# Performance work log

Hardware: AMD Instinct MI355X
Metric: run time of the kernel (lower is better)

The kernel has to match this reference:

```python
import jax, jax.numpy as jnp
import numpy as np

D_MODEL = 512
HIDDEN = 2 * D_MODEL
B, L = 8, 2048
R_MIN, R_MAX = 0.8, 0.99
LN_EPS = 1e-5


def setup_inputs() -> dict:
    key = jax.random.key(0)
    ks = jax.random.split(key, 12)
    x = jax.random.normal(ks[0], (B, L, D_MODEL), jnp.float32)
    mask = jnp.ones((B, L), jnp.float32)
    # LRU eigenvalue init, exactly as the torch __init__
    u1 = jax.random.uniform(ks[1], (HIDDEN,), jnp.float32)
    u2 = jax.random.uniform(ks[2], (HIDDEN,), jnp.float32)
    nu_log = jnp.log(-0.5 * jnp.log(u1 * (R_MAX ** 2 - R_MIN ** 2) + R_MIN ** 2))
    theta_log = jnp.log(u2 * 2.0 * np.pi)
    diag_lambda = jnp.exp(jax.lax.complex(-jnp.exp(nu_log), jnp.exp(theta_log)))
    gamma_log = jnp.log(jnp.sqrt(1.0 - jnp.abs(diag_lambda) ** 2))
    params_log = jnp.stack([nu_log, theta_log, gamma_log])  # (3, HIDDEN)
    s_in = 1.0 / np.sqrt(D_MODEL)
    s_out = 1.0 / np.sqrt(HIDDEN)
    # complex Linear weights (real+imag parts; trained weights are fully complex)
    W_in_re = jax.random.uniform(ks[3], (HIDDEN, D_MODEL), jnp.float32, -s_in, s_in)
    W_in_im = jax.random.uniform(ks[4], (HIDDEN, D_MODEL), jnp.float32, -s_in, s_in)
    b_in_re = jax.random.uniform(ks[5], (HIDDEN,), jnp.float32, -s_in, s_in)
    b_in_im = jax.random.uniform(ks[6], (HIDDEN,), jnp.float32, -s_in, s_in)
    W_out_re = jax.random.uniform(ks[7], (D_MODEL, HIDDEN), jnp.float32, -s_out, s_out)
    W_out_im = jax.random.uniform(ks[8], (D_MODEL, HIDDEN), jnp.float32, -s_out, s_out)
    b_out_re = jax.random.uniform(ks[9], (D_MODEL,), jnp.float32, -s_out, s_out)
    b_out_im = jax.random.uniform(ks[10], (D_MODEL,), jnp.float32, -s_out, s_out)
    ln_w = jnp.ones((D_MODEL,), jnp.float32)
    ln_b = jnp.zeros((D_MODEL,), jnp.float32)
    return dict(x=x, mask=mask, params_log=params_log,
                W_in_re=W_in_re, W_in_im=W_in_im, b_in_re=b_in_re, b_in_im=b_in_im,
                W_out_re=W_out_re, W_out_im=W_out_im, b_out_re=b_out_re, b_out_im=b_out_im,
                ln_w=ln_w, ln_b=ln_b)


def _lru_parallel_scan(h, lamb, mask, Bn, Ln, Dn):
    # log-depth doubling trick over complex diagonal recurrence (faithful port)
    log2_L = int(np.ceil(np.log2(Ln)))
    for i in range(1, log2_L + 1):
        l = 2 ** i
        h = h.reshape(Bn * Ln // l, l, Dn)
        m = mask.reshape(Bn * Ln // l, l)
        h1, h2 = h[:, : l // 2], h[:, l // 2 :]
        if i > 1:
            lamb = jnp.concatenate([lamb, lamb * lamb[-1]], axis=0)  # powers lam^1..lam^(l/2)
        h2 = h2 + lamb * h1[:, -1:] * m[:, l // 2 - 1 : l // 2, None]
        h = jnp.concatenate([h1, h2], axis=1)
    return h.reshape(Bn, Ln, Dn)


def reference(x, mask, params_log, W_in_re, W_in_im, b_in_re, b_in_im,
              W_out_re, W_out_im, b_out_re, b_out_im, ln_w, ln_b):
    nu, theta, gamma = jnp.exp(params_log)  # each (HIDDEN,)
    lamb = jnp.exp(jax.lax.complex(-nu, theta))[None, :]  # (1, HIDDEN)
    W_in = jax.lax.complex(W_in_re, W_in_im)
    b_in = jax.lax.complex(b_in_re, b_in_im)
    W_out = jax.lax.complex(W_out_re, W_out_im)
    b_out = jax.lax.complex(b_out_re, b_out_im)
    xc = x.astype(jnp.complex64)
    h = (jnp.einsum('bld,hd->blh', xc, W_in) + b_in) * gamma  # (B, L, HIDDEN) complex64
    Bn, Ln, Dn = h.shape
    h = _lru_parallel_scan(h, lamb, mask, Bn, Ln, Dn)
    y = (jnp.einsum('blh,dh->bld', h, W_out) + b_out).real + x  # dropout = identity (eval)
    mean = jnp.mean(y, axis=-1, keepdims=True)
    var = jnp.var(y, axis=-1, keepdims=True)
    return (y - mean) / jnp.sqrt(var + LN_EPS) * ln_w + ln_b
```

## Files before the change

kernel.cpp:

```cpp
#include <hip/hip_runtime.h>
#include <hip/hip_bf16.h>
#include <cstdint>
#include <cstddef>


typedef unsigned short u16;
typedef __attribute__((ext_vector_type(8))) short bf16x8;
typedef __attribute__((ext_vector_type(4))) float f32x4;

#define B_    8
#define L_    2048
#define D_    512
#define H_    1024
#define M_    (B_ * L_)
#define SEG_  32
#define T_    (L_ / SEG_)

__device__ __forceinline__ float b2f(u16 u) {
  union { unsigned int i; float f; } v; v.i = ((unsigned int)u) << 16; return v.f;
}
__device__ __forceinline__ u16 f2b(float f) {
  union { float f; unsigned int i; } v; v.f = f;
  unsigned int x = v.i;
  return (u16)((x + 0x7fffu + ((x >> 16) & 1u)) >> 16);
}

__device__ __forceinline__ void gl2lds16(const void* g, void* l) {
  __builtin_amdgcn_global_load_lds(
      (const __attribute__((address_space(1))) void*)g,
      (__attribute__((address_space(3))) void*)l, 16, 0, 0);
}

__device__ __forceinline__ int ksw(int row, int kc) {
  return (kc ^ (row & 3) ^ ((row >> 2) & 3)) & 3;
}

__global__ __launch_bounds__(256) void conv_f32_bf16(
    const float* __restrict__ in, u16* __restrict__ out, int n4)
{
  int i = blockIdx.x * 256 + threadIdx.x;
  if (i < n4) {
    float4 v = ((const float4*)in)[i];
    ushort4 o;
    o.x = f2b(v.x); o.y = f2b(v.y); o.z = f2b(v.z); o.w = f2b(v.w);
    ((ushort4*)out)[i] = o;
  }
}

__global__ __launch_bounds__(256) void prep_wcat(
    const float* __restrict__ wre, const float* __restrict__ wim,
    u16* __restrict__ wcat)
{
  int i = blockIdx.x * 256 + threadIdx.x;
  int d = i >> 10, c = i & 1023;
  wcat[(size_t)d * 2048 + c]        = f2b(wre[i]);
  wcat[(size_t)d * 2048 + 1024 + c] = f2b(-wim[i]);
}

template <int MODE>
__global__ __launch_bounds__(256, 2) void gemm_bt(
    const u16* __restrict__ A, const u16* __restrict__ Bp, int K,
    void* __restrict__ outp, int ldc,
    const float* __restrict__ p0, const float* __restrict__ p1,
    const float* __restrict__ p2)
{
  __shared__ __align__(16) u16 sA[128 * 32];
  __shared__ __align__(16) u16 sB[128 * 32];

  const int tid  = threadIdx.x;
  const int lane = tid & 63;
  const int wave = tid >> 6;
  const int wm = wave >> 1, wn = wave & 1;
  const int m0 = blockIdx.y * 128;
  const int n0 = blockIdx.x * 128;

  f32x4 acc[4][4];
#pragma unroll
  for (int i = 0; i < 4; ++i)
#pragma unroll
    for (int j = 0; j < 4; ++j) { f32x4 z = {0.f, 0.f, 0.f, 0.f}; acc[i][j] = z; }

  const int q = lane >> 4;
  const int r = lane & 15;

  for (int k0 = 0; k0 < K; k0 += 32) {
#pragma unroll
    for (int it = 0; it < 2; ++it) {
      int ci  = it * 256 + tid;
      int row = ci >> 2;
      int kc  = ksw(row, ci & 3);
      gl2lds16(A  + (size_t)(m0 + row) * K + k0 + kc * 8, &sA[ci * 8]);
      gl2lds16(Bp + (size_t)(n0 + row) * K + k0 + kc * 8, &sB[ci * 8]);
    }
    __syncthreads();

    bf16x8 af[4], bfv[4];
#pragma unroll
    for (int mt = 0; mt < 4; ++mt) {
      int arow = wm * 64 + mt * 16 + r;
      int slot = (arow << 2) | ksw(arow, q);
      af[mt] = *(const bf16x8*)&sA[slot * 8];
    }
#pragma unroll
    for (int nt = 0; nt < 4; ++nt) {
      int brow = wn * 64 + nt * 16 + r;
      int slot = (brow << 2) | ksw(brow, q);
      bfv[nt] = *(const bf16x8*)&sB[slot * 8];
    }
#pragma unroll
    for (int mt = 0; mt < 4; ++mt)
#pragma unroll
      for (int nt = 0; nt < 4; ++nt)
        acc[mt][nt] = __builtin_amdgcn_mfma_f32_16x16x32_bf16(
            af[mt], bfv[nt], acc[mt][nt], 0, 0, 0);
    __syncthreads();
  }

#pragma unroll
  for (int nt = 0; nt < 4; ++nt) {
    const int ng = n0 + wn * 64 + nt * 16 + r;
    float bias, gam = 1.f;
    if (MODE == 0) {
      bias = (ng < 1024) ? p0[ng] : p1[ng - 1024];
      gam  = expf(p2[2 * H_ + (ng & (H_ - 1))]);
    } else {
      bias = p0[ng];
    }
#pragma unroll
    for (int mt = 0; mt < 4; ++mt) {
      const int mg = m0 + wm * 64 + mt * 16 + q * 4;
#pragma unroll
      for (int i = 0; i < 4; ++i) {
        float v = acc[mt][nt][i] + bias;
        if (MODE == 0)
          ((u16*)outp)[(size_t)(mg + i) * ldc + ng] = f2b(v * gam);
        else
          ((float*)outp)[(size_t)(mg + i) * ldc + ng] = v;
      }
    }
  }
}

__global__ __launch_bounds__(256) void scan_local(
    u16* __restrict__ h, const float* __restrict__ mask,
    const float* __restrict__ params, float2* __restrict__ segfin,
    float* __restrict__ prodm)
{
  const int s = blockIdx.x, b = blockIdx.y;
  const int c4 = threadIdx.x * 4;
  float lr[4], li[4];
#pragma unroll
  for (int j = 0; j < 4; ++j) {
    int c = c4 + j;
    float nu = expf(params[c]);
    float th = expf(params[H_ + c]);
    float mg = expf(-nu);
    lr[j] = mg * cosf(th);
    li[j] = mg * sinf(th);
  }
  const int t0 = s * T_;
  u16* p = h + (size_t)(b * L_ + t0) * (2 * H_) + c4;
  const float* mp = mask + b * L_ + t0;
  float sr[4] = {0, 0, 0, 0}, si[4] = {0, 0, 0, 0};
  float pm = 1.f;
  ushort4 cre = *(const ushort4*)p;
  ushort4 cim = *(const ushort4*)(p + H_);
  for (int i = 0; i < T_; ++i) {
    ushort4 nre = cre, nim = cim;
    if (i + 1 < T_) {
      nre = *(const ushort4*)(p + 2 * H_);
      nim = *(const ushort4*)(p + 2 * H_ + H_);
    }
    float fac = (t0 + i == 0) ? 0.f : mp[i - 1];
    pm *= fac;
    u16 rr[4], ii[4], orr[4], oii[4];
    *(ushort4*)rr = cre; *(ushort4*)ii = cim;
#pragma unroll
    for (int j = 0; j < 4; ++j) {
      float ar = fac * sr[j], ai = fac * si[j];
      float nr2 = b2f(rr[j]) + lr[j] * ar - li[j] * ai;
      float ni2 = b2f(ii[j]) + lr[j] * ai + li[j] * ar;
      sr[j] = nr2; si[j] = ni2;
      orr[j] = f2b(nr2); oii[j] = f2b(ni2);
    }
    *(ushort4*)p        = *(ushort4*)orr;
    *(ushort4*)(p + H_) = *(ushort4*)oii;
    p += 2 * H_;
    cre = nre; cim = nim;
  }
#pragma unroll
  for (int j = 0; j < 4; ++j)
    segfin[(size_t)(b * SEG_ + s) * H_ + c4 + j] = make_float2(sr[j], si[j]);
  if (threadIdx.x == 0) prodm[b * SEG_ + s] = pm;
}

__global__ __launch_bounds__(256) void scan_carry(
    const float2* __restrict__ segfin, const float* __restrict__ prodm,
    const float* __restrict__ params, float2* __restrict__ carries)
{
  int idx = blockIdx.x * 256 + threadIdx.x;
  int b = idx >> 10, c = idx & 1023;
  float nu = expf(params[c]);
  float th = expf(params[H_ + c]);
  float mg = expf(-nu * (float)T_);
  float ltr = mg * cosf(th * (float)T_);
  float lti = mg * sinf(th * (float)T_);
  float cr = 0.f, ci = 0.f;
  for (int s = 0; s < SEG_; ++s) {
    size_t o = (size_t)(b * SEG_ + s) * H_ + c;
    carries[o] = make_float2(cr, ci);
    float2 fin = segfin[o];
    float pmv = prodm[b * SEG_ + s];
    float nr = fin.x + pmv * (ltr * cr - lti * ci);
    float ni = fin.y + pmv * (ltr * ci + lti * cr);
    cr = nr; ci = ni;
  }
}

__global__ __launch_bounds__(256) void scan_apply(
    u16* __restrict__ h, const float* __restrict__ mask,
    const float* __restrict__ params, const float2* __restrict__ carries)
{
  const int s = blockIdx.x + 1, b = blockIdx.y;
  const int c4 = threadIdx.x * 4;
  float lr[4], li[4], cr[4], ci[4];
#pragma unroll
  for (int j = 0; j < 4; ++j) {
    int c = c4 + j;
    float nu = expf(params[c]);
    float th = expf(params[H_ + c]);
    float mg = expf(-nu);
    lr[j] = mg * cosf(th);
    li[j] = mg * sinf(th);
    float2 cv = carries[(size_t)(b * SEG_ + s) * H_ + c];
    cr[j] = cv.x; ci[j] = cv.y;
  }
  const int t0 = s * T_;
  u16* p = h + (size_t)(b * L_ + t0) * (2 * H_) + c4;
  const float* mp = mask + b * L_ + t0;
  for (int i = 0; i < T_; ++i) {
    float fac = mp[i - 1];
    u16 rr[4], ii[4], orr[4], oii[4];
    *(ushort4*)rr = *(const ushort4*)p;
    *(ushort4*)ii = *(const ushort4*)(p + H_);
#pragma unroll
    for (int j = 0; j < 4; ++j) {
      float nr2 = fac * (lr[j] * cr[j] - li[j] * ci[j]);
      float ni2 = fac * (lr[j] * ci[j] + li[j] * cr[j]);
      cr[j] = nr2; ci[j] = ni2;
      orr[j] = f2b(b2f(rr[j]) + nr2);
      oii[j] = f2b(b2f(ii[j]) + ni2);
    }
    *(ushort4*)p        = *(ushort4*)orr;
    *(ushort4*)(p + H_) = *(ushort4*)oii;
    p += 2 * H_;
  }
}

__global__ __launch_bounds__(256) void ln_kernel(
    const float* __restrict__ y, const float* __restrict__ xg,
    const float* __restrict__ lnw, const float* __restrict__ lnb,
    float* __restrict__ out)
{
  const int wave = threadIdx.x >> 6, lane = threadIdx.x & 63;
  const size_t row = (size_t)blockIdx.x * 4 + wave;
  const float* yr = y + row * 512;
  const float* xr = xg + row * 512;
  float z[8];
  { float4 t = *(const float4*)&yr[lane * 4];        z[0]=t.x; z[1]=t.y; z[2]=t.z; z[3]=t.w; }
  { float4 t = *(const float4*)&yr[256 + lane * 4];  z[4]=t.x; z[5]=t.y; z[6]=t.z; z[7]=t.w; }
  { float4 t = *(const float4*)&xr[lane * 4];        z[0]+=t.x; z[1]+=t.y; z[2]+=t.z; z[3]+=t.w; }
  { float4 t = *(const float4*)&xr[256 + lane * 4];  z[4]+=t.x; z[5]+=t.y; z[6]+=t.z; z[7]+=t.w; }
  float s = 0.f, ss = 0.f;
#pragma unroll
  for (int j = 0; j < 8; ++j) { s += z[j]; ss += z[j] * z[j]; }
#pragma unroll
  for (int o = 32; o > 0; o >>= 1) { s += __shfl_xor(s, o); ss += __shfl_xor(ss, o); }
  const float mean = s * (1.f / 512.f);
  const float var  = ss * (1.f / 512.f) - mean * mean;
  const float inv  = rsqrtf(var + 1e-5f);
  float ov[8];
#pragma unroll
  for (int j = 0; j < 8; ++j) {
    int col = (j < 4) ? (lane * 4 + j) : (256 + lane * 4 + (j - 4));
    ov[j] = (z[j] - mean) * inv * lnw[col] + lnb[col];
  }
  { float4 t; t.x=ov[0]; t.y=ov[1]; t.z=ov[2]; t.w=ov[3];
    *(float4*)&out[row * 512 + lane * 4] = t; }
  { float4 t; t.x=ov[4]; t.y=ov[5]; t.z=ov[6]; t.w=ov[7];
    *(float4*)&out[row * 512 + 256 + lane * 4] = t; }
}

extern "C" void kernel_launch(void* const* d_in, const int* in_sizes, int n_in,
                              void* d_out, int out_size, void* d_ws, size_t ws_size,
                              hipStream_t stream) {
  (void)in_sizes; (void)n_in; (void)out_size; (void)ws_size;
  const float* x      = (const float*)d_in[0];
  const float* mask   = (const float*)d_in[1];
  const float* params = (const float*)d_in[2];
  const float* Wire   = (const float*)d_in[3];
  const float* Wiim   = (const float*)d_in[4];
  const float* bire   = (const float*)d_in[5];
  const float* biim   = (const float*)d_in[6];
  const float* Wore   = (const float*)d_in[7];
  const float* Woim   = (const float*)d_in[8];
  const float* bore   = (const float*)d_in[9];
  const float* lnw    = (const float*)d_in[11];
  const float* lnb    = (const float*)d_in[12];

  char* ws = (char*)d_ws;
  float*  y       = (float*) (ws);
  u16*    xb      = (u16*)   (ws);
  u16*    h       = (u16*)   (ws + (size_t)33554432);
  u16*    winb    = (u16*)   (ws + (size_t)100663296);
  u16*    wcat    = (u16*)   (ws + (size_t)102760448);
  float2* segfin  = (float2*)(ws + (size_t)104857600);
  float2* carries = (float2*)(ws + (size_t)106954752);
  float*  prodm   = (float*) (ws + (size_t)109051904);

  conv_f32_bf16<<<8192, 256, 0, stream>>>(x, xb, M_ * D_ / 4);
  conv_f32_bf16<<<512, 256, 0, stream>>>(Wire, winb, H_ * D_ / 4);
  conv_f32_bf16<<<512, 256, 0, stream>>>(Wiim, winb + H_ * D_, H_ * D_ / 4);
  prep_wcat<<<2048, 256, 0, stream>>>(Wore, Woim, wcat);

  gemm_bt<0><<<dim3(16, 128), 256, 0, stream>>>(
      xb, winb, 512, (void*)h, 2048, bire, biim, params);

  scan_local<<<dim3(SEG_, B_), 256, 0, stream>>>(h, mask, params, segfin, prodm);
  scan_carry<<<32, 256, 0, stream>>>(segfin, prodm, params, carries);
  scan_apply<<<dim3(SEG_ - 1, B_), 256, 0, stream>>>(h, mask, params, carries);

  gemm_bt<1><<<dim3(4, 128), 256, 0, stream>>>(
      h, wcat, 2048, (void*)y, 512, bore, nullptr, nullptr);

  ln_kernel<<<4096, 256, 0, stream>>>(y, x, lnw, lnb, (float*)d_out);
}
```

Baseline: 288.8 us.

## Restructure LRU scan into read-only segment pass plus full rescan, double segments

The first scan pass now only reads h (no write-back) to compute segment final states, using an unrolled double-buffered prefetch of 8 rows at a time. The second pass reruns the full recurrence from the carry and writes h once, so h is written in a single pass instead of twice. SEG is doubled to 64 for more blocks, and the segment-power lambda^T is computed by repeated squaring. Other changes: weight prep is merged into one kernel, the GEMM grid order is swapped so M varies fastest, and launch bounds are raised to 4 blocks per CU, which may increase register pressure.

```diff
diff --git a/kernel.cpp b/kernel.cpp
--- a/kernel.cpp
+++ b/kernel.cpp
@@ -13,7 +13,7 @@
 #define D_    512
 #define H_    1024
 #define M_    (B_ * L_)
-#define SEG_  32
+#define SEG_  64
 #define T_    (L_ / SEG_)
 
 __device__ __forceinline__ float b2f(u16 u) {
@@ -47,18 +47,21 @@
   }
 }
 
-__global__ __launch_bounds__(256) void prep_wcat(
-    const float* __restrict__ wre, const float* __restrict__ wim,
-    u16* __restrict__ wcat)
+__global__ __launch_bounds__(256) void prep_weights(
+    const float* __restrict__ wire, const float* __restrict__ wiim,
+    const float* __restrict__ wore, const float* __restrict__ woim,
+    u16* __restrict__ winb, u16* __restrict__ wcat)
 {
   int i = blockIdx.x * 256 + threadIdx.x;
+  winb[i]                  = f2b(wire[i]);
+  winb[H_ * D_ + i]        = f2b(wiim[i]);
   int d = i >> 10, c = i & 1023;
-  wcat[(size_t)d * 2048 + c]        = f2b(wre[i]);
-  wcat[(size_t)d * 2048 + 1024 + c] = f2b(-wim[i]);
+  wcat[(size_t)d * 2048 + c]        = f2b(wore[i]);
+  wcat[(size_t)d * 2048 + 1024 + c] = f2b(-woim[i]);
 }
 
 template <int MODE>
-__global__ __launch_bounds__(256, 2) void gemm_bt(
+__global__ __launch_bounds__(256, 4) void gemm_bt(
     const u16* __restrict__ A, const u16* __restrict__ Bp, int K,
     void* __restrict__ outp, int ldc,
     const float* __restrict__ p0, const float* __restrict__ p1,
@@ -71,8 +74,8 @@
   const int lane = tid & 63;
   const int wave = tid >> 6;
   const int wm = wave >> 1, wn = wave & 1;
-  const int m0 = blockIdx.y * 128;
-  const int n0 = blockIdx.x * 128;
+  const int m0 = blockIdx.x * 128;
+  const int n0 = blockIdx.y * 128;
 
   f32x4 acc[4][4];
 #pragma unroll
@@ -141,8 +144,8 @@
   }
 }
 
-__global__ __launch_bounds__(256) void scan_local(
-    u16* __restrict__ h, const float* __restrict__ mask,
+__global__ __launch_bounds__(256) void scan_fin(
+    const u16* __restrict__ h, const float* __restrict__ mask,
     const float* __restrict__ params, float2* __restrict__ segfin,
     float* __restrict__ prodm)
 {
@@ -159,34 +162,44 @@
     li[j] = mg * sinf(th);
   }
   const int t0 = s * T_;
-  u16* p = h + (size_t)(b * L_ + t0) * (2 * H_) + c4;
+  const u16* p = h + (size_t)(b * L_ + t0) * (2 * H_) + c4;
   const float* mp = mask + b * L_ + t0;
+  float fac0;
+  if (t0 == 0) fac0 = 0.f; else fac0 = mask[b * L_ + t0 - 1];
+
+  ushort4 bre[2][8], bim[2][8];
+#pragma unroll
+  for (int j = 0; j < 8; ++j) {
+    bre[0][j] = *(const ushort4*)(p + (size_t)j * 2 * H_);
+    bim[0][j] = *(const ushort4*)(p + (size_t)j * 2 * H_ + H_);
+  }
   float sr[4] = {0, 0, 0, 0}, si[4] = {0, 0, 0, 0};
   float pm = 1.f;
-  ushort4 cre = *(const ushort4*)p;
-  ushort4 cim = *(const ushort4*)(p + H_);
-  for (int i = 0; i < T_; ++i) {
-    ushort4 nre = cre, nim = cim;
-    if (i + 1 < T_) {
-      nre = *(const ushort4*)(p + 2 * H_);
-      nim = *(const ushort4*)(p + 2 * H_ + H_);
-    }
-    float fac = (t0 + i == 0) ? 0.f : mp[i - 1];
-    pm *= fac;
-    u16 rr[4], ii[4], orr[4], oii[4];
-    *(ushort4*)rr = cre; *(ushort4*)ii = cim;
-#pragma unroll
-    for (int j = 0; j < 4; ++j) {
-      float ar = fac * sr[j], ai = fac * si[j];
-      float nr2 = b2f(rr[j]) + lr[j] * ar - li[j] * ai;
-      float ni2 = b2f(ii[j]) + lr[j] * ai + li[j] * ar;
-      sr[j] = nr2; si[j] = ni2;
-      orr[j] = f2b(nr2); oii[j] = f2b(ni2);
-    }
-    *(ushort4*)p        = *(ushort4*)orr;
-    *(ushort4*)(p + H_) = *(ushort4*)oii;
-    p += 2 * H_;
-    cre = nre; cim = nim;
+#pragma unroll
+  for (int ch = 0; ch < T_ / 8; ++ch) {
+    const int cur = ch & 1, nxt = cur ^ 1;
+    if (ch < T_ / 8 - 1) {
+      const u16* pn = p + (size_t)(ch + 1) * 8 * 2 * H_;
+#pragma unroll
+      for (int j = 0; j < 8; ++j) {
+        bre[nxt][j] = *(const ushort4*)(pn + (size_t)j * 2 * H_);
+        bim[nxt][j] = *(const ushort4*)(pn + (size_t)j * 2 * H_ + H_);
+      }
+    }
+#pragma unroll
+    for (int j = 0; j < 8; ++j) {
+      int i = ch * 8 + j;
+      float fac = (i == 0) ? fac0 : mp[i - 1];
+      pm *= fac;
+      u16 rr[4], ii[4];
+      *(ushort4*)rr = bre[cur][j]; *(ushort4*)ii = bim[cur][j];
+#pragma unroll
+      for (int k = 0; k < 4; ++k) {
+        float ar = fac * sr[k], ai = fac * si[k];
+        sr[k] = b2f(rr[k]) + lr[k] * ar - li[k] * ai;
+        si[k] = b2f(ii[k]) + lr[k] * ai + li[k] * ar;
+      }
+    }
   }
 #pragma unroll
   for (int j = 0; j < 4; ++j)
@@ -202,9 +215,14 @@
   int b = idx >> 10, c = idx & 1023;
   float nu = expf(params[c]);
   float th = expf(params[H_ + c]);
-  float mg = expf(-nu * (float)T_);
-  float ltr = mg * cosf(th * (float)T_);
-  float lti = mg * sinf(th * (float)T_);
+  float mg = expf(-nu);
+  float ltr = mg * cosf(th), lti = mg * sinf(th);
+#pragma unroll
+  for (int sq = 0; sq < 5; ++sq) {
+    float nr = ltr * ltr - lti * lti;
+    float ni = 2.f * ltr * lti;
+    ltr = nr; lti = ni;
+  }
   float cr = 0.f, ci = 0.f;
   for (int s = 0; s < SEG_; ++s) {
     size_t o = (size_t)(b * SEG_ + s) * H_ + c;
@@ -217,13 +235,13 @@
   }
 }
 
-__global__ __launch_bounds__(256) void scan_apply(
+__global__ __launch_bounds__(256) void scan_full(
     u16* __restrict__ h, const float* __restrict__ mask,
     const float* __restrict__ params, const float2* __restrict__ carries)
 {
-  const int s = blockIdx.x + 1, b = blockIdx.y;
+  const int s = blockIdx.x, b = blockIdx.y;
   const int c4 = threadIdx.x * 4;
-  float lr[4], li[4], cr[4], ci[4];
+  float lr[4], li[4], sr[4], si[4];
 #pragma unroll
   for (int j = 0; j < 4; ++j) {
     int c = c4 + j;
@@ -233,27 +251,37 @@
     lr[j] = mg * cosf(th);
     li[j] = mg * sinf(th);
     float2 cv = carries[(size_t)(b * SEG_ + s) * H_ + c];
-    cr[j] = cv.x; ci[j] = cv.y;
+    sr[j] = cv.x; si[j] = cv.y;
   }
   const int t0 = s * T_;
   u16* p = h + (size_t)(b * L_ + t0) * (2 * H_) + c4;
   const float* mp = mask + b * L_ + t0;
+  float fac0;
+  if (t0 == 0) fac0 = 0.f; else fac0 = mask[b * L_ + t0 - 1];
+
+  ushort4 cre = *(const ushort4*)p;
+  ushort4 cim = *(const ushort4*)(p + H_);
   for (int i = 0; i < T_; ++i) {
-    float fac = mp[i - 1];
+    ushort4 nre = cre, nim = cim;
+    if (i + 1 < T_) {
+      nre = *(const ushort4*)(p + 2 * H_);
+      nim = *(const ushort4*)(p + 2 * H_ + H_);
+    }
+    float fac = (i == 0) ? fac0 : mp[i - 1];
     u16 rr[4], ii[4], orr[4], oii[4];
-    *(ushort4*)rr = *(const ushort4*)p;
-    *(ushort4*)ii = *(const ushort4*)(p + H_);
+    *(ushort4*)rr = cre; *(ushort4*)ii = cim;
 #pragma unroll
     for (int j = 0; j < 4; ++j) {
-      float nr2 = fac * (lr[j] * cr[j] - li[j] * ci[j]);
-      float ni2 = fac * (lr[j] * ci[j] + li[j] * cr[j]);
-      cr[j] = nr2; ci[j] = ni2;
-      orr[j] = f2b(b2f(rr[j]) + nr2);
-      oii[j] = f2b(b2f(ii[j]) + ni2);
+      float ar = fac * sr[j], ai = fac * si[j];
+      float nr2 = b2f(rr[j]) + lr[j] * ar - li[j] * ai;
+      float ni2 = b2f(ii[j]) + lr[j] * ai + li[j] * ar;
+      sr[j] = nr2; si[j] = ni2;
+      orr[j] = f2b(nr2); oii[j] = f2b(ni2);
     }
     *(ushort4*)p        = *(ushort4*)orr;
     *(ushort4*)(p + H_) = *(ushort4*)oii;
     p += 2 * H_;
+    cre = nre; cim = nim;
   }
 }
 
@@ -309,28 +337,26 @@
   const float* lnb    = (const float*)d_in[12];
 
   char* ws = (char*)d_ws;
+  u16*    xb      = (u16*)   (ws);
+  float2* segfin  = (float2*)(ws);
+  float2* carries = (float2*)(ws + (size_t)4194304);
+  float*  prodm   = (float*) (ws + (size_t)8388608);
   float*  y       = (float*) (ws);
-  u16*    xb      = (u16*)   (ws);
   u16*    h       = (u16*)   (ws + (size_t)33554432);
   u16*    winb    = (u16*)   (ws + (size_t)100663296);
   u16*    wcat    = (u16*)   (ws + (size_t)102760448);
-  float2* segfin  = (float2*)(ws + (size_t)104857600);
-  float2* carries = (float2*)(ws + (size_t)106954752);
-  float*  prodm   = (float*) (ws + (size_t)109051904);
 
   conv_f32_bf16<<<8192, 256, 0, stream>>>(x, xb, M_ * D_ / 4);
-  conv_f32_bf16<<<512, 256, 0, stream>>>(Wire, winb, H_ * D_ / 4);
-  conv_f32_bf16<<<512, 256, 0, stream>>>(Wiim, winb + H_ * D_, H_ * D_ / 4);
-  prep_wcat<<<2048, 256, 0, stream>>>(Wore, Woim, wcat);
-
-  gemm_bt<0><<<dim3(16, 128), 256, 0, stream>>>(
+  prep_weights<<<2048, 256, 0, stream>>>(Wire, Wiim, Wore, Woim, winb, wcat);
+
+  gemm_bt<0><<<dim3(128, 16), 256, 0, stream>>>(
       xb, winb, 512, (void*)h, 2048, bire, biim, params);
 
-  scan_local<<<dim3(SEG_, B_), 256, 0, stream>>>(h, mask, params, segfin, prodm);
+  scan_fin<<<dim3(SEG_, B_), 256, 0, stream>>>(h, mask, params, segfin, prodm);
   scan_carry<<<32, 256, 0, stream>>>(segfin, prodm, params, carries);
-  scan_apply<<<dim3(SEG_ - 1, B_), 256, 0, stream>>>(h, mask, params, carries);
-
-  gemm_bt<1><<<dim3(4, 128), 256, 0, stream>>>(
+  scan_full<<<dim3(SEG_, B_), 256, 0, stream>>>(h, mask, params, carries);
+
+  gemm_bt<1><<<dim3(128, 4), 256, 0, stream>>>(
       h, wcat, 2048, (void*)y, 512, bore, nullptr, nullptr);
 
   ln_kernel<<<4096, 256, 0, stream>>>(y, x, lnw, lnb, (float*)d_out);
```

Result: faster. 262.5 us (-9.1%).
